# Optimization experiments

Measured on AMD Instinct MI355X. Metric: run time of the kernel, lower is better.

## Reference

```python
import jax, jax.numpy as jnp
import numpy as np

WIN = 7
DIM = 384
HEADS = 12
HEAD_DIM = DIM // HEADS


def relative_position_index(win):
    ch = np.arange(win)
    cw = np.arange(win)
    coords = np.stack(np.meshgrid(ch, cw, indexing='ij'))  # [2,w,w]
    cf = coords.reshape(2, -1)
    rel = cf[:, :, None] - cf[:, None, :]  # [2,ww,ww]
    rel = rel.transpose(1, 2, 0)
    rel[:, :, 0] += win - 1
    rel[:, :, 1] += win - 1
    rel[:, :, 0] *= 2 * win - 1
    return jnp.array(rel.sum(-1), dtype=jnp.int32)  # [ww,ww]


def setup_inputs() -> dict:
    key = jax.random.key(0)
    ks = jax.random.split(key, 9)
    B, S = 1024, WIN * WIN
    M = 16  # windows per image
    s = 1.0 / np.sqrt(DIM)
    return {
        'hidden_states': jax.random.normal(ks[0], (B, S, DIM), jnp.float32),
        'attention_mask': jax.random.normal(ks[1], (M, S, S), jnp.float32),
        'Wq': jax.random.normal(ks[2], (DIM, DIM), jnp.float32) * s,
        'bq': jnp.zeros((DIM,), jnp.float32),
        'Wk': jax.random.normal(ks[3], (DIM, DIM), jnp.float32) * s,
        'bk': jnp.zeros((DIM,), jnp.float32),
        'Wv': jax.random.normal(ks[4], (DIM, DIM), jnp.float32) * s,
        'bv': jnp.zeros((DIM,), jnp.float32),
        'rel_bias_table': jax.random.normal(ks[5], ((2 * WIN - 1) ** 2, HEADS), jnp.float32) * 0.02,
        'rel_index': relative_position_index(WIN),
    }


def reference(hidden_states, attention_mask, Wq, bq, Wk, bk, Wv, bv, rel_bias_table, rel_index):
    B, S, _ = hidden_states.shape
    q = (hidden_states @ Wq + bq).reshape(B, S, HEADS, HEAD_DIM)
    k = (hidden_states @ Wk + bk).reshape(B, S, HEADS, HEAD_DIM)
    v = (hidden_states @ Wv + bv).reshape(B, S, HEADS, HEAD_DIM)
    q = q / jnp.sqrt(jnp.float32(HEAD_DIM)).astype(q.dtype)
    attn = jnp.einsum('bqhd,bkhd->bhqk', q, k)  # [B,H,S,S]
    # relative position bias: gather + reshape + transpose -> [1,H,S,S]
    bias = rel_bias_table[rel_index.reshape(-1)].reshape(S, S, HEADS)
    attn = attn + jnp.transpose(bias, (2, 0, 1))[None]
    # shifted-window mask add: [B//M, M, H, S, S]
    Mw = attention_mask.shape[0]
    attn = attn.reshape(B // Mw, Mw, HEADS, S, S) + attention_mask[None, :, None, :, :]
    attn = attn.reshape(B, HEADS, S, S)
    attn = jax.nn.softmax(attn, axis=-1)
    out = jnp.einsum('bhqk,bkhd->bqhd', attn, v).reshape(B, S, DIM)
    return out
```

## Files before the change

kernel.cpp:

```cpp
#include <hip/hip_runtime.h>

typedef __attribute__((ext_vector_type(8))) short short8;
typedef __attribute__((ext_vector_type(4))) float f32x4;
typedef __attribute__((ext_vector_type(4))) int i32x4;

__device__ __forceinline__ unsigned short f2bf(float f) {
  unsigned u = __builtin_bit_cast(unsigned, f);
  u += 0x7fffu + ((u >> 16) & 1u);
  return (unsigned short)(u >> 16);
}

#define GLOAD_LDS16(g, l)                                                              \
  __builtin_amdgcn_global_load_lds(                                                    \
      (const __attribute__((address_space(1))) unsigned int*)(g),                      \
      (__attribute__((address_space(3))) unsigned int*)(l), 16, 0, 0)

__global__ __launch_bounds__(256) void k_convert(const float* __restrict__ x,
                                                 unsigned short* __restrict__ y) {
  int i = blockIdx.x * 256 + threadIdx.x;
  const float* p = x + (size_t)i * 8;
  f32x4 a = *(const f32x4*)p;
  f32x4 b = *(const f32x4*)(p + 4);
  short8 v;
  v[0] = (short)f2bf(a[0]); v[1] = (short)f2bf(a[1]); v[2] = (short)f2bf(a[2]); v[3] = (short)f2bf(a[3]);
  v[4] = (short)f2bf(b[0]); v[5] = (short)f2bf(b[1]); v[6] = (short)f2bf(b[2]); v[7] = (short)f2bf(b[3]);
  *(short8*)(y + (size_t)i * 8) = v;
}

__global__ __launch_bounds__(256) void k_prepw(const float* __restrict__ Wq, const float* __restrict__ Wk,
                                               const float* __restrict__ Wv, const float* __restrict__ bq,
                                               const float* __restrict__ bk, const float* __restrict__ bv,
                                               unsigned short* __restrict__ Wt, float* __restrict__ bvec) {
  int i = blockIdx.x * 256 + threadIdx.x;
  int n = i / 384, k = i - n * 384;
  int which = n / 384;
  int c = n - which * 384;
  const float* W = (which == 0) ? Wq : (which == 1) ? Wk : Wv;
  Wt[i] = f2bf(W[k * 384 + c]);
  if (k == 0) {
    const float* bb = (which == 0) ? bq : (which == 1) ? bk : bv;
    bvec[n] = bb[c];
  }
}

__global__ __launch_bounds__(256) void k_prept(const float* __restrict__ tab, const int* __restrict__ ridx,
                                               const float* __restrict__ am, float* __restrict__ T) {
  int i = blockIdx.x * 256 + threadIdx.x;
  int lane = i & 63;
  int rest = i >> 6;
  int ik = rest & 3, jq = (rest >> 2) & 3, wh = rest >> 4;
  int h = wh % 12, w = wh / 12;
  int lr = lane & 15, lg = lane >> 4;
  int q = jq * 16 + lr;
  f32x4 v;
  #pragma unroll
  for (int r = 0; r < 4; ++r) {
    int k = ik * 16 + lg * 4 + r;
    v[r] = (q < 49 && k < 49) ? tab[ridx[q * 49 + k] * 12 + h] + am[w * 2401 + q * 49 + k] : 0.f;
  }
  *(f32x4*)(T + (size_t)i * 4) = v;
}

__global__ __launch_bounds__(256) void k_qkv(const unsigned short* __restrict__ X,
                                             const unsigned short* __restrict__ Wt,
                                             const float* __restrict__ bvec,
                                             unsigned short* __restrict__ Qo,
                                             unsigned short* __restrict__ Ko,
                                             unsigned short* __restrict__ Vo) {
  __shared__ __align__(16) unsigned short As[128 * 64];
  __shared__ __align__(16) unsigned short Bs[128 * 64];
  int orig = blockIdx.x;
  int wg = (orig & 7) * 441 + (orig >> 3);
  int bm = wg / 9, bn = wg - (wg / 9) * 9;
  int tid = threadIdx.x;
  int lane = tid & 63, wid = tid >> 6;
  int trow = tid >> 3, tcc = tid & 7;
  const unsigned short* Ag = X + (size_t)(bm * 128) * 384;
  const unsigned short* Bg = Wt + (size_t)(bn * 128) * 384;
  int moff = (wid >> 1) * 64, noff = (wid & 1) * 64;
  int lrow = lane & 15, lgrp = lane >> 4;
  char* AsB = (char*)As + (size_t)wid * 1024;
  char* BsB = (char*)Bs + (size_t)wid * 1024;
  f32x4 acc[4][4] = {};
  for (int ks = 0; ks < 6; ++ks) {
    __syncthreads();
    #pragma unroll
    for (int c = 0; c < 4; ++c) {
      int row = trow + 32 * c;
      int colsw = 8 * (tcc ^ (row & 7)) + ks * 64;
      GLOAD_LDS16(Ag + (size_t)row * 384 + colsw, AsB + c * 4096);
      GLOAD_LDS16(Bg + (size_t)row * 384 + colsw, BsB + c * 4096);
    }
    __syncthreads();
    #pragma unroll
    for (int hh = 0; hh < 2; ++hh) {
      short8 a[4], b[4];
      #pragma unroll
      for (int i = 0; i < 4; ++i) {
        int ra = moff + i * 16 + lrow;
        a[i] = *(const short8*)&As[ra * 64 + ((lgrp + 4 * hh) ^ (ra & 7)) * 8];
        int rb = noff + i * 16 + lrow;
        b[i] = *(const short8*)&Bs[rb * 64 + ((lgrp + 4 * hh) ^ (rb & 7)) * 8];
      }
      #pragma unroll
      for (int i = 0; i < 4; ++i)
        #pragma unroll
        for (int j = 0; j < 4; ++j)
          acc[i][j] = __builtin_amdgcn_mfma_f32_16x16x32_bf16(a[i], b[j], acc[i][j], 0, 0, 0);
    }
  }
  int which = bn / 3;
  unsigned short* Dst = (which == 0) ? Qo : (which == 1) ? Ko : Vo;
  int nbase = bn * 128 - which * 384;
  float scale = (which == 0) ? 0.17677669529663687f : 1.0f;
  #pragma unroll
  for (int i = 0; i < 4; ++i) {
    #pragma unroll
    for (int j2 = 0; j2 < 4; ++j2) {
      int row = moff + i * 16 + lgrp * 4 + j2;
      int gm = bm * 128 + row;
      int bb = gm / 49, ss = gm - bb * 49;
      #pragma unroll
      for (int j = 0; j < 4; ++j) {
        int n = nbase + noff + j * 16 + lrow;
        int h = n >> 5, d = n & 31;
        float val = (acc[i][j][j2] + bvec[which * 384 + n]) * scale;
        Dst[((size_t)(bb * 12 + h) * 49 + ss) * 32 + d] = f2bf(val);
      }
    }
  }
}

__global__ __launch_bounds__(64) void k_attn(const unsigned short* __restrict__ Qb,
                                             const unsigned short* __restrict__ Kb,
                                             const unsigned short* __restrict__ Vb,
                                             const float* __restrict__ T,
                                             float* __restrict__ out) {
  __shared__ __align__(16) unsigned short Ps[64 * 64];
  __shared__ __align__(16) unsigned short Vt[32 * 72];
  int bh = blockIdx.x;
  int b = bh / 12, h = bh - b * 12;
  int lane = threadIdx.x;
  int lr = lane & 15, lg = lane >> 4;
  const unsigned short* Qg = Qb + (size_t)bh * 1568;
  const unsigned short* Kg = Kb + (size_t)bh * 1568;
  const unsigned short* Vg = Vb + (size_t)bh * 1568;

  short8 z = {0, 0, 0, 0, 0, 0, 0, 0};
  short8 vreg[4];
  #pragma unroll
  for (int it = 0; it < 4; ++it) {
    int c = lane + 64 * it;
    int r = c >> 2, c8 = (c & 3) * 8;
    vreg[it] = (r < 49) ? *(const short8*)(Vg + r * 32 + c8) : z;
  }
  short8 qf[4], kf[4];
  #pragma unroll
  for (int t = 0; t < 4; ++t) {
    int rq = t * 16 + lr; if (rq > 48) rq = 48;
    qf[t] = *(const short8*)(Qg + rq * 32 + lg * 8);
    kf[t] = *(const short8*)(Kg + rq * 32 + lg * 8);
  }
  f32x4 sc[4][4] = {};
  #pragma unroll
  for (int ik = 0; ik < 4; ++ik)
    #pragma unroll
    for (int jq = 0; jq < 4; ++jq)
      sc[ik][jq] = __builtin_amdgcn_mfma_f32_16x16x32_bf16(kf[ik], qf[jq], sc[ik][jq], 0, 0, 0);

  #pragma unroll
  for (int it = 0; it < 4; ++it) {
    int c = lane + 64 * it;
    int r = c >> 2, c8 = (c & 3) * 8;
    #pragma unroll
    for (int j = 0; j < 8; ++j) Vt[(c8 + j) * 72 + r] = (unsigned short)vreg[it][j];
  }

  const float* Tb = T + ((size_t)((b & 15) * 12 + h)) * 4096;
  #pragma unroll
  for (int jq = 0; jq < 4; ++jq) {
    #pragma unroll
    for (int ik = 0; ik < 4; ++ik) {
      f32x4 tv = *(const f32x4*)(Tb + ((jq * 4 + ik) * 64 + lane) * 4);
      #pragma unroll
      for (int r = 0; r < 4; ++r) {
        float v = sc[ik][jq][r] + tv[r];
        if (ik == 3) {
          if (r == 0) v = (lg == 0) ? v : -1e30f;
          else v = -1e30f;
        }
        sc[ik][jq][r] = v;
      }
    }
    float m = -1e30f;
    #pragma unroll
    for (int ik = 0; ik < 4; ++ik)
      #pragma unroll
      for (int r = 0; r < 4; ++r) m = fmaxf(m, sc[ik][jq][r]);
    m = fmaxf(m, __shfl_xor(m, 16));
    m = fmaxf(m, __shfl_xor(m, 32));
    float s = 0.f;
    #pragma unroll
    for (int ik = 0; ik < 4; ++ik)
      #pragma unroll
      for (int r = 0; r < 4; ++r) {
        float e = __expf(sc[ik][jq][r] - m);
        sc[ik][jq][r] = e;
        s += e;
      }
    s += __shfl_xor(s, 16);
    s += __shfl_xor(s, 32);
    float iv = 1.0f / s;
    int q = jq * 16 + lr;
    #pragma unroll
    for (int ik = 0; ik < 4; ++ik) {
      unsigned d0 = (unsigned)f2bf(sc[ik][jq][0] * iv) | ((unsigned)f2bf(sc[ik][jq][1] * iv) << 16);
      unsigned d1 = (unsigned)f2bf(sc[ik][jq][2] * iv) | ((unsigned)f2bf(sc[ik][jq][3] * iv) << 16);
      unsigned off = (unsigned)(q * 128 + ik * 32 + lg * 8) ^ ((unsigned)(lr & 7) << 4);
      *(uint2*)((char*)Ps + off) = make_uint2(d0, d1);
    }
  }
  __syncthreads();

  short8 vf[2][2];
  #pragma unroll
  for (int kk = 0; kk < 2; ++kk)
    #pragma unroll
    for (int nl = 0; nl < 2; ++nl)
      vf[kk][nl] = *(const short8*)&Vt[(nl * 16 + lr) * 72 + kk * 32 + lg * 8];
  f32x4 ao[4][2] = {};
  #pragma unroll
  for (int i = 0; i < 4; ++i) {
    short8 pf[2];
    #pragma unroll
    for (int kk = 0; kk < 2; ++kk) {
      unsigned off = (unsigned)((i * 16 + lr) * 128 + (kk * 4 + lg) * 16) ^ ((unsigned)(lr & 7) << 4);
      pf[kk] = *(const short8*)((char*)Ps + off);
    }
    #pragma unroll
    for (int nl = 0; nl < 2; ++nl)
      #pragma unroll
      for (int kk = 0; kk < 2; ++kk)
        ao[i][nl] = __builtin_amdgcn_mfma_f32_16x16x32_bf16(pf[kk], vf[kk][nl], ao[i][nl], 0, 0, 0);
  }

  #pragma unroll
  for (int i = 0; i < 4; ++i) {
    #pragma unroll
    for (int j2 = 0; j2 < 4; ++j2) {
      int q = i * 16 + lg * 4 + j2;
      if (q < 49) {
        #pragma unroll
        for (int nl = 0; nl < 2; ++nl) {
          int d = nl * 16 + lr;
          out[((size_t)(b * 49 + q)) * 384 + h * 32 + d] = ao[i][nl][j2];
        }
      }
    }
  }
}

extern "C" void kernel_launch(void* const* d_in, const int* in_sizes, int n_in,
                              void* d_out, int out_size, void* d_ws, size_t ws_size,
                              hipStream_t stream) {
  const float* hs  = (const float*)d_in[0];
  const float* am  = (const float*)d_in[1];
  const float* Wq  = (const float*)d_in[2];
  const float* bq  = (const float*)d_in[3];
  const float* Wk  = (const float*)d_in[4];
  const float* bk  = (const float*)d_in[5];
  const float* Wv  = (const float*)d_in[6];
  const float* bv  = (const float*)d_in[7];
  const float* tab = (const float*)d_in[8];
  const int*   rix = (const int*)d_in[9];
  float* out = (float*)d_out;
  char* ws = (char*)d_ws;

  size_t o = 0;
  auto alloc = [&](size_t bytes) { size_t r = o; o = (o + bytes + 255) & ~(size_t)255; return r; };
  unsigned short* Xb   = (unsigned short*)(ws + alloc(50176ull * 384 * 2));
  unsigned short* Wt   = (unsigned short*)(ws + alloc(1152ull * 384 * 2));
  float*          bvec = (float*)(ws + alloc(1152ull * 4));
  float*          Tt   = (float*)(ws + alloc(192ull * 4096 * 4));
  unsigned short* Qb   = (unsigned short*)(ws + alloc(19267584ull * 2));
  unsigned short* Kb   = (unsigned short*)(ws + alloc(19267584ull * 2));
  unsigned short* Vb   = (unsigned short*)(ws + alloc(19267584ull * 2));
  (void)ws_size; (void)in_sizes; (void)n_in; (void)out_size;

  k_convert<<<9408, 256, 0, stream>>>(hs, Xb);
  k_prepw<<<1728, 256, 0, stream>>>(Wq, Wk, Wv, bq, bk, bv, Wt, bvec);
  k_prept<<<768, 256, 0, stream>>>(tab, rix, am, Tt);
  k_qkv<<<3528, 256, 0, stream>>>(Xb, Wt, bvec, Qb, Kb, Vb);
  k_attn<<<12288, 64, 0, stream>>>(Qb, Kb, Vb, Tt, out);
}
```

Baseline: 262.5 us.

## Fuse input conversion, QKV projection and window attention into one kernel

Measured after the change: 282.7 us. 7.7% more time.

```diff
diff --git a/kernel.cpp b/kernel.cpp
--- a/kernel.cpp
+++ b/kernel.cpp
@@ -8,23 +8,6 @@
   unsigned u = __builtin_bit_cast(unsigned, f);
   u += 0x7fffu + ((u >> 16) & 1u);
   return (unsigned short)(u >> 16);
-}
-
-#define GLOAD_LDS16(g, l)                                                              \
-  __builtin_amdgcn_global_load_lds(                                                    \
-      (const __attribute__((address_space(1))) unsigned int*)(g),                      \
-      (__attribute__((address_space(3))) unsigned int*)(l), 16, 0, 0)
-
-__global__ __launch_bounds__(256) void k_convert(const float* __restrict__ x,
-                                                 unsigned short* __restrict__ y) {
-  int i = blockIdx.x * 256 + threadIdx.x;
-  const float* p = x + (size_t)i * 8;
-  f32x4 a = *(const f32x4*)p;
-  f32x4 b = *(const f32x4*)(p + 4);
-  short8 v;
-  v[0] = (short)f2bf(a[0]); v[1] = (short)f2bf(a[1]); v[2] = (short)f2bf(a[2]); v[3] = (short)f2bf(a[3]);
-  v[4] = (short)f2bf(b[0]); v[5] = (short)f2bf(b[1]); v[6] = (short)f2bf(b[2]); v[7] = (short)f2bf(b[3]);
-  *(short8*)(y + (size_t)i * 8) = v;
 }
 
 __global__ __launch_bounds__(256) void k_prepw(const float* __restrict__ Wq, const float* __restrict__ Wk,
@@ -61,105 +44,112 @@
   *(f32x4*)(T + (size_t)i * 4) = v;
 }
 
-__global__ __launch_bounds__(256) void k_qkv(const unsigned short* __restrict__ X,
-                                             const unsigned short* __restrict__ Wt,
-                                             const float* __restrict__ bvec,
-                                             unsigned short* __restrict__ Qo,
-                                             unsigned short* __restrict__ Ko,
-                                             unsigned short* __restrict__ Vo) {
-  __shared__ __align__(16) unsigned short As[128 * 64];
-  __shared__ __align__(16) unsigned short Bs[128 * 64];
-  int orig = blockIdx.x;
-  int wg = (orig & 7) * 441 + (orig >> 3);
-  int bm = wg / 9, bn = wg - (wg / 9) * 9;
-  int tid = threadIdx.x;
-  int lane = tid & 63, wid = tid >> 6;
-  int trow = tid >> 3, tcc = tid & 7;
-  const unsigned short* Ag = X + (size_t)(bm * 128) * 384;
-  const unsigned short* Bg = Wt + (size_t)(bn * 128) * 384;
-  int moff = (wid >> 1) * 64, noff = (wid & 1) * 64;
-  int lrow = lane & 15, lgrp = lane >> 4;
-  char* AsB = (char*)As + (size_t)wid * 1024;
-  char* BsB = (char*)Bs + (size_t)wid * 1024;
-  f32x4 acc[4][4] = {};
-  for (int ks = 0; ks < 6; ++ks) {
-    __syncthreads();
-    #pragma unroll
-    for (int c = 0; c < 4; ++c) {
-      int row = trow + 32 * c;
-      int colsw = 8 * (tcc ^ (row & 7)) + ks * 64;
-      GLOAD_LDS16(Ag + (size_t)row * 384 + colsw, AsB + c * 4096);
-      GLOAD_LDS16(Bg + (size_t)row * 384 + colsw, BsB + c * 4096);
-    }
-    __syncthreads();
-    #pragma unroll
-    for (int hh = 0; hh < 2; ++hh) {
-      short8 a[4], b[4];
-      #pragma unroll
-      for (int i = 0; i < 4; ++i) {
-        int ra = moff + i * 16 + lrow;
-        a[i] = *(const short8*)&As[ra * 64 + ((lgrp + 4 * hh) ^ (ra & 7)) * 8];
-        int rb = noff + i * 16 + lrow;
-        b[i] = *(const short8*)&Bs[rb * 64 + ((lgrp + 4 * hh) ^ (rb & 7)) * 8];
-      }
-      #pragma unroll
-      for (int i = 0; i < 4; ++i)
+__global__ __launch_bounds__(768, 3) void k_mega(const float* __restrict__ X,
+                                                 const unsigned short* __restrict__ Wt,
+                                                 const float* __restrict__ bvec,
+                                                 const float* __restrict__ T,
+                                                 float* __restrict__ out) {
+  extern __shared__ unsigned short pool[];
+  const int w = blockIdx.x;
+  const int tid = threadIdx.x;
+  const int lane = tid & 63, wid = tid >> 6;
+  const int lr = lane & 15, lg = lane >> 4;
+  char* poolB = (char*)pool;
+
+  #pragma unroll
+  for (int it = 0; it < 4; ++it) {
+    int c = tid + 768 * it;
+    int row = c / 48, c8 = c - row * 48;
+    short8 v = {0, 0, 0, 0, 0, 0, 0, 0};
+    if (row < 49) {
+      const float* p = X + ((size_t)(w * 49 + row)) * 384 + c8 * 8;
+      f32x4 f0 = *(const f32x4*)p;
+      f32x4 f1 = *(const f32x4*)(p + 4);
+      v[0] = (short)f2bf(f0[0]); v[1] = (short)f2bf(f0[1]); v[2] = (short)f2bf(f0[2]); v[3] = (short)f2bf(f0[3]);
+      v[4] = (short)f2bf(f1[0]); v[5] = (short)f2bf(f1[1]); v[6] = (short)f2bf(f1[2]); v[7] = (short)f2bf(f1[3]);
+    }
+    *(short8*)(poolB + row * 768 + ((c8 * 16) ^ ((row & 7) << 4))) = v;
+  }
+  __syncthreads();
+
+  const unsigned swz = (unsigned)((lr & 7) << 4);
+  unsigned hq[16], hk[16], hv[16];
+  auto gemm_pass = [&](int p, float scl, unsigned* hd) {
+    f32x4 acc[4][2] = {};
+    const unsigned short* Bg = Wt + ((size_t)(p * 384 + wid * 32 + lr)) * 384;
+    short8 aC[4], bC[2], aN[4], bN[2];
+    #pragma unroll
+    for (int mi = 0; mi < 4; ++mi)
+      aC[mi] = *(const short8*)(poolB + (16 * mi + lr) * 768 + (unsigned)((0 + lg * 16) ^ swz));
+    bC[0] = *(const short8*)(Bg + lg * 8);
+    bC[1] = *(const short8*)(Bg + 16 * 384 + lg * 8);
+    #pragma unroll 2
+    for (int k = 0; k < 12; ++k) {
+      if (k < 11) {
         #pragma unroll
-        for (int j = 0; j < 4; ++j)
-          acc[i][j] = __builtin_amdgcn_mfma_f32_16x16x32_bf16(a[i], b[j], acc[i][j], 0, 0, 0);
-    }
-  }
-  int which = bn / 3;
-  unsigned short* Dst = (which == 0) ? Qo : (which == 1) ? Ko : Vo;
-  int nbase = bn * 128 - which * 384;
-  float scale = (which == 0) ? 0.17677669529663687f : 1.0f;
-  #pragma unroll
-  for (int i = 0; i < 4; ++i) {
-    #pragma unroll
-    for (int j2 = 0; j2 < 4; ++j2) {
-      int row = moff + i * 16 + lgrp * 4 + j2;
-      int gm = bm * 128 + row;
-      int bb = gm / 49, ss = gm - bb * 49;
-      #pragma unroll
-      for (int j = 0; j < 4; ++j) {
-        int n = nbase + noff + j * 16 + lrow;
-        int h = n >> 5, d = n & 31;
-        float val = (acc[i][j][j2] + bvec[which * 384 + n]) * scale;
-        Dst[((size_t)(bb * 12 + h) * 49 + ss) * 32 + d] = f2bf(val);
-      }
-    }
-  }
-}
-
-__global__ __launch_bounds__(64) void k_attn(const unsigned short* __restrict__ Qb,
-                                             const unsigned short* __restrict__ Kb,
-                                             const unsigned short* __restrict__ Vb,
-                                             const float* __restrict__ T,
-                                             float* __restrict__ out) {
-  __shared__ __align__(16) unsigned short Ps[64 * 64];
-  __shared__ __align__(16) unsigned short Vt[32 * 72];
-  int bh = blockIdx.x;
-  int b = bh / 12, h = bh - b * 12;
-  int lane = threadIdx.x;
-  int lr = lane & 15, lg = lane >> 4;
-  const unsigned short* Qg = Qb + (size_t)bh * 1568;
-  const unsigned short* Kg = Kb + (size_t)bh * 1568;
-  const unsigned short* Vg = Vb + (size_t)bh * 1568;
-
-  short8 z = {0, 0, 0, 0, 0, 0, 0, 0};
-  short8 vreg[4];
-  #pragma unroll
-  for (int it = 0; it < 4; ++it) {
-    int c = lane + 64 * it;
-    int r = c >> 2, c8 = (c & 3) * 8;
-    vreg[it] = (r < 49) ? *(const short8*)(Vg + r * 32 + c8) : z;
-  }
+        for (int mi = 0; mi < 4; ++mi)
+          aN[mi] = *(const short8*)(poolB + (16 * mi + lr) * 768 + (unsigned)(((k + 1) * 64 + lg * 16) ^ swz));
+        bN[0] = *(const short8*)(Bg + (k + 1) * 32 + lg * 8);
+        bN[1] = *(const short8*)(Bg + 16 * 384 + (k + 1) * 32 + lg * 8);
+      }
+      #pragma unroll
+      for (int mi = 0; mi < 4; ++mi)
+        #pragma unroll
+        for (int ni = 0; ni < 2; ++ni)
+          acc[mi][ni] = __builtin_amdgcn_mfma_f32_16x16x32_bf16(aC[mi], bC[ni], acc[mi][ni], 0, 0, 0);
+      #pragma unroll
+      for (int mi = 0; mi < 4; ++mi) aC[mi] = aN[mi];
+      bC[0] = bN[0]; bC[1] = bN[1];
+    }
+    float b0 = bvec[p * 384 + wid * 32 + lr];
+    float b1 = bvec[p * 384 + wid * 32 + 16 + lr];
+    #pragma unroll
+    for (int mi = 0; mi < 4; ++mi)
+      #pragma unroll
+      for (int ni = 0; ni < 2; ++ni) {
+        float bb = ni ? b1 : b0;
+        float v0 = (acc[mi][ni][0] + bb) * scl;
+        float v1 = (acc[mi][ni][1] + bb) * scl;
+        float v2 = (acc[mi][ni][2] + bb) * scl;
+        float v3 = (acc[mi][ni][3] + bb) * scl;
+        hd[(mi * 2 + ni) * 2 + 0] = (unsigned)f2bf(v0) | ((unsigned)f2bf(v1) << 16);
+        hd[(mi * 2 + ni) * 2 + 1] = (unsigned)f2bf(v2) | ((unsigned)f2bf(v3) << 16);
+      }
+  };
+  gemm_pass(0, 0.17677669529663687f, hq);
+  gemm_pass(1, 1.0f, hk);
+  gemm_pass(2, 1.0f, hv);
+  __syncthreads();
+
+  unsigned short* reg = pool + wid * 6400;
+  unsigned short* Qs = reg;
+  unsigned short* Ks = reg + 1984;
+  unsigned short* Vt = reg + 4096;
+  char* Pb = (char*)reg;
+  #pragma unroll
+  for (int mi = 0; mi < 4; ++mi)
+    #pragma unroll
+    for (int ni = 0; ni < 2; ++ni)
+      #pragma unroll
+      for (int r = 0; r < 4; ++r) {
+        int s = 16 * mi + 4 * lg + r;
+        int d = ni * 16 + lr;
+        unsigned short qv = (unsigned short)(hq[(mi * 2 + ni) * 2 + (r >> 1)] >> ((r & 1) * 16));
+        unsigned short kv = (unsigned short)(hk[(mi * 2 + ni) * 2 + (r >> 1)] >> ((r & 1) * 16));
+        unsigned short vv = (unsigned short)(hv[(mi * 2 + ni) * 2 + (r >> 1)] >> ((r & 1) * 16));
+        if (s < 49) {
+          Qs[s * 40 + d] = qv;
+          Ks[s * 40 + d] = kv;
+        }
+        Vt[d * 72 + s] = vv;
+      }
+
   short8 qf[4], kf[4];
   #pragma unroll
   for (int t = 0; t < 4; ++t) {
     int rq = t * 16 + lr; if (rq > 48) rq = 48;
-    qf[t] = *(const short8*)(Qg + rq * 32 + lg * 8);
-    kf[t] = *(const short8*)(Kg + rq * 32 + lg * 8);
+    qf[t] = *(const short8*)&Qs[rq * 40 + lg * 8];
+    kf[t] = *(const short8*)&Ks[rq * 40 + lg * 8];
   }
   f32x4 sc[4][4] = {};
   #pragma unroll
@@ -168,15 +158,7 @@
     for (int jq = 0; jq < 4; ++jq)
       sc[ik][jq] = __builtin_amdgcn_mfma_f32_16x16x32_bf16(kf[ik], qf[jq], sc[ik][jq], 0, 0, 0);
 
-  #pragma unroll
-  for (int it = 0; it < 4; ++it) {
-    int c = lane + 64 * it;
-    int r = c >> 2, c8 = (c & 3) * 8;
-    #pragma unroll
-    for (int j = 0; j < 8; ++j) Vt[(c8 + j) * 72 + r] = (unsigned short)vreg[it][j];
-  }
-
-  const float* Tb = T + ((size_t)((b & 15) * 12 + h)) * 4096;
+  const float* Tb = T + ((size_t)((w & 15) * 12 + wid)) * 4096;
   #pragma unroll
   for (int jq = 0; jq < 4; ++jq) {
     #pragma unroll
@@ -217,10 +199,9 @@
       unsigned d0 = (unsigned)f2bf(sc[ik][jq][0] * iv) | ((unsigned)f2bf(sc[ik][jq][1] * iv) << 16);
       unsigned d1 = (unsigned)f2bf(sc[ik][jq][2] * iv) | ((unsigned)f2bf(sc[ik][jq][3] * iv) << 16);
       unsigned off = (unsigned)(q * 128 + ik * 32 + lg * 8) ^ ((unsigned)(lr & 7) << 4);
-      *(uint2*)((char*)Ps + off) = make_uint2(d0, d1);
-    }
-  }
-  __syncthreads();
+      *(uint2*)(Pb + off) = make_uint2(d0, d1);
+    }
+  }
 
   short8 vf[2][2];
   #pragma unroll
@@ -235,7 +216,7 @@
     #pragma unroll
     for (int kk = 0; kk < 2; ++kk) {
       unsigned off = (unsigned)((i * 16 + lr) * 128 + (kk * 4 + lg) * 16) ^ ((unsigned)(lr & 7) << 4);
-      pf[kk] = *(const short8*)((char*)Ps + off);
+      pf[kk] = *(const short8*)(Pb + off);
     }
     #pragma unroll
     for (int nl = 0; nl < 2; ++nl)
@@ -253,7 +234,7 @@
         #pragma unroll
         for (int nl = 0; nl < 2; ++nl) {
           int d = nl * 16 + lr;
-          out[((size_t)(b * 49 + q)) * 384 + h * 32 + d] = ao[i][nl][j2];
+          out[((size_t)(w * 49 + q)) * 384 + wid * 32 + d] = ao[i][nl][j2];
         }
       }
     }
@@ -278,18 +259,16 @@
 
   size_t o = 0;
   auto alloc = [&](size_t bytes) { size_t r = o; o = (o + bytes + 255) & ~(size_t)255; return r; };
-  unsigned short* Xb   = (unsigned short*)(ws + alloc(50176ull * 384 * 2));
   unsigned short* Wt   = (unsigned short*)(ws + alloc(1152ull * 384 * 2));
   float*          bvec = (float*)(ws + alloc(1152ull * 4));
   float*          Tt   = (float*)(ws + alloc(192ull * 4096 * 4));
-  unsigned short* Qb   = (unsigned short*)(ws + alloc(19267584ull * 2));
-  unsigned short* Kb   = (unsigned short*)(ws + alloc(19267584ull * 2));
-  unsigned short* Vb   = (unsigned short*)(ws + alloc(19267584ull * 2));
   (void)ws_size; (void)in_sizes; (void)n_in; (void)out_size;
 
-  k_convert<<<9408, 256, 0, stream>>>(hs, Xb);
+  static int lds_set = 0;
+  (void)lds_set;
+  hipFuncSetAttribute((const void*)k_mega, hipFuncAttributeMaxDynamicSharedMemorySize, 153600);
+
   k_prepw<<<1728, 256, 0, stream>>>(Wq, Wk, Wv, bq, bk, bv, Wt, bvec);
   k_prept<<<768, 256, 0, stream>>>(tab, rix, am, Tt);
-  k_qkv<<<3528, 256, 0, stream>>>(Xb, Wt, bvec, Qb, Kb, Vb);
-  k_attn<<<12288, 64, 0, stream>>>(Qb, Kb, Vb, Tt, out);
-}
+  k_mega<<<1024, 768, 153600, stream>>>(hs, Wt, bvec, Tt, out);
+}
```
